# Kernel optimization log

Hardware: AMD Instinct MI355X
Metric: run time of the kernel (lower is better)

The kernel has to match this reference:

```python
import math
import jax, jax.numpy as jnp
import numpy as np

HEAD_DIM = 64


def skew(X):
    # X: (B, M, L). Pad M+1 zeros on last dim, flatten, drop last M, reshape.
    # Shifts row i right by i -> aligns relative positions (adaptive-span trick).
    B, M, L = X.shape
    X = jnp.pad(X, ((0, 0), (0, 0), (0, M + 1)))  # (B, M, L+M+1)
    X = X.reshape(B, -1)[:, :-M].reshape(B, M, M + L)
    return X


def setup_inputs() -> dict:
    key = jax.random.key(0)
    k1, k2, k3, k4 = jax.random.split(key, 4)
    BH, M, D, LIM = 16, 2048, HEAD_DIM, 2048
    return {
        "query": jax.random.normal(k1, (BH, M, D), jnp.float32),
        "key": jax.random.normal(k2, (BH, M, D), jnp.float32),
        "value": jax.random.normal(k3, (BH, M, D), jnp.float32),
        "key_pe": jax.random.normal(k4, (1, D, LIM), jnp.float32),
    }


def reference(query, key, value, key_pe):
    M = query.shape[1]
    Lk = key.shape[1]
    neg_inf = jnp.float32(float("-inf"))
    # causal mask: -inf strictly above diagonal, last M rows
    mask_causal = jnp.triu(jnp.full((Lk, Lk), neg_inf, dtype=query.dtype), k=1)[-M:]
    # content scores: (BH, M, Lk)
    attn = jnp.einsum("bmd,bld->bml", query, key)
    L_size = attn.shape[-1]
    # relative-position scores via skew trick
    attn_pos = jnp.einsum("bmd,xdl->bml", query, key_pe[:, :, -L_size:])
    attn_pos = skew(attn_pos)[:, :, -L_size - 1:-1]
    attn = (attn + attn_pos + mask_causal) / math.sqrt(HEAD_DIM)
    attn = jax.nn.softmax(attn, axis=-1)
    out = jnp.einsum("bml,bld->bmd", attn, value)
    return out  # aux_loss is the constant 0 in the original module
```

## Files before the change

kernel.cpp:

```cpp
#include <hip/hip_runtime.h>
#include <hip/hip_bf16.h>

typedef __attribute__((ext_vector_type(8))) short short8;
typedef __attribute__((ext_vector_type(4))) float f32x4;

#define MFMA16(A, B, C) __builtin_amdgcn_mfma_f32_16x16x32_bf16((A), (B), (C), 0, 0, 0)

#define GL16(gp, lp) __builtin_amdgcn_global_load_lds( \
    (const __attribute__((address_space(1))) void*)(gp), \
    (__attribute__((address_space(3))) void*)(lp), 16, 0, 0)

__device__ __forceinline__ unsigned short bfbits(float f) {
  return __builtin_bit_cast(unsigned short, (__bf16)f);
}

constexpr int BH = 16;
constexpr int Mn = 2048;
constexpr int Dn = 64;
constexpr int LIMn = 2048;
constexpr size_t KF_SHORTS = (size_t)BH * 32 * 8 * 512;
constexpr size_t PE_JROWS = 132;
constexpr size_t PEF_SHORTS = PE_JROWS * 2 * 512;
constexpr int PART_SLOT = 4224;
constexpr int SLOTS_PER_HEAD = 72;

__device__ __forceinline__ int part_offs(int mt) {
  return (mt < 16) ? 2 * (mt - 8) : (mt < 24 ? 16 + 3 * (mt - 16) : 40 + 4 * (mt - 24));
}


__global__ void prep_all(const float* __restrict__ K, const float* __restrict__ V,
                         const float* __restrict__ PE,
                         unsigned short* __restrict__ Kf, unsigned short* __restrict__ Vf,
                         unsigned short* __restrict__ PEf) {
  __shared__ float tA[64 * 64];
  __shared__ float tB[64 * 64];
  const int b = blockIdx.x, tid = threadIdx.x;
  const int w = tid >> 6, lane = tid & 63, g = lane >> 4, q15 = lane & 15;

  if (b < 512) {
    const int bh = b >> 5, lt = b & 31;
    const float* Ks = K + ((size_t)bh * Mn + lt * 64) * Dn;
    const float* Vs = V + ((size_t)bh * Mn + lt * 64) * Dn;
    const int row = tid >> 2, c0 = (tid & 3) * 16;
#pragma unroll
    for (int i = 0; i < 4; ++i) {
      *(float4*)&tA[row * 64 + c0 + 4 * i] = ((const float4*)(Ks + (size_t)row * 64 + c0))[i];
      *(float4*)&tB[row * 64 + c0 + 4 * i] = ((const float4*)(Vs + (size_t)row * 64 + c0))[i];
    }
    __syncthreads();
#pragma unroll
    for (int i = 0; i < 2; ++i) {
      const int f = 2 * w + i, nt = f >> 1, s = f & 1;
      short8 uk, uv;
#pragma unroll
      for (int j = 0; j < 8; ++j) {
        uk[j] = (short)bfbits(tA[(nt * 16 + q15) * 64 + s * 32 + g * 8 + j]);
        uv[j] = (short)bfbits(tB[(s * 32 + g * 8 + j) * 64 + nt * 16 + q15]);
      }
      const size_t base = ((size_t)(bh * 32 + lt) * 8 + f) * 512 + lane * 8;
      *(short8*)&Kf[base] = uk;
      *(short8*)&Vf[base] = uv;
    }
  } else {
    const int pb = b - 512;
    const int c0 = pb * 64;
    const int d = tid >> 2, cc = (tid & 3) * 16;
#pragma unroll
    for (int i = 0; i < 16; ++i) {
      const int c = c0 + cc + i;
      tA[(cc + i) * 64 + d] = (c < LIMn) ? PE[(size_t)d * LIMn + c] : 0.0f;
    }
    __syncthreads();
#pragma unroll
    for (int s = 0; s < 2; ++s) {
      short8 u;
#pragma unroll
      for (int j = 0; j < 8; ++j)
        u[j] = (short)bfbits(tA[(w * 16 + q15) * 64 + s * 32 + g * 8 + j]);
      *(short8*)&PEf[((size_t)(4 * pb + w) * 2 + s) * 512 + lane * 8] = u;
    }
  }
}


__launch_bounds__(256)
__global__ void stair_main(const float* __restrict__ Qg,
                           const unsigned short* __restrict__ Kf,
                           const unsigned short* __restrict__ Vf,
                           const unsigned short* __restrict__ PEf,
                           float* __restrict__ Og,
                           float* __restrict__ Part,
                           int split) {
  __shared__ __align__(16) unsigned short Kbuf[2][2][4096];
  __shared__ __align__(16) unsigned short Vbuf[2][2][4096];
  __shared__ __align__(16) unsigned short Plds[4][2048];

  const int tid = threadIdx.x;
  const int w = tid >> 6, lane = tid & 63, g = lane >> 4, q15 = lane & 15;
  const int bid = blockIdx.x;

  int bh, mt, chunk, t0, t1, nch;
  bh = bid & 15;
  if (split) {
    const int u = bid >> 4;
    if (u < 32)      { mt = 31 - (u >> 2); chunk = u & 3; }
    else if (u < 56) { const int v = u - 32, q = v / 3; mt = 23 - q; chunk = v - q * 3; }
    else if (u < 72) { const int v = u - 56; mt = 15 - (v >> 1); chunk = v & 1; }
    else             { mt = 7 - (u - 72); chunk = 0; }
    t0 = chunk * 8;
    t1 = (t0 + 8 < mt + 1) ? (t0 + 8) : (mt + 1);
    nch = (mt + 8) >> 3;
  } else {
    mt = 31 - (bid >> 4); chunk = 0; t0 = 0; t1 = mt + 1; nch = 1;
  }
  const int m0w = mt * 64 + w * 16;

  const float* Qb = Qg + (size_t)bh * Mn * Dn;
  float* Ob = Og + (size_t)bh * Mn * Dn;

  short8 aq[2];
  {
    const float* qp = Qb + (size_t)(m0w + q15) * Dn;
#pragma unroll
    for (int s = 0; s < 2; ++s) {
      const float4* p = (const float4*)(qp + s * 32 + g * 8);
      float4 f0 = p[0], f1 = p[1];
      short8 a;
      a[0]=(short)bfbits(f0.x); a[1]=(short)bfbits(f0.y); a[2]=(short)bfbits(f0.z); a[3]=(short)bfbits(f0.w);
      a[4]=(short)bfbits(f1.x); a[5]=(short)bfbits(f1.y); a[6]=(short)bfbits(f1.z); a[7]=(short)bfbits(f1.w);
      aq[s] = a;
    }
  }

  float mrun[4], lrun[4];
  f32x4 o[4] = {};
#pragma unroll
  for (int r = 0; r < 4; ++r) { mrun[r] = -1e30f; lrun[r] = 0.0f; }

  auto STAGE1 = [&](int b, int slot, int t) {
    const size_t toff = ((size_t)(bh * 32 + t) * 8) * 512;
#pragma unroll
    for (int i = 0; i < 2; ++i) {
      const int f = 2 * w + i;
      const size_t off = toff + (size_t)f * 512 + lane * 8;
      GL16(&Kf[off], &Kbuf[b][slot][f * 512]);
      GL16(&Vf[off], &Vbuf[b][slot][f * 512]);
    }
  };

  auto QK = [&](f32x4 qk[4], int cur, int slot, int ntmax) {
#pragma unroll
    for (int s = 0; s < 2; ++s)
#pragma unroll
      for (int nt = 0; nt < 4; ++nt)
        if (nt <= ntmax) {
          short8 bfr = *(const short8*)&Kbuf[cur][slot][(nt * 2 + s) * 512 + lane * 8];
          qk[nt] = MFMA16(aq[s], bfr, qk[nt]);
        }
  };

  auto GATHER = [&](float sv[4][4], const f32x4 qk[4], const f32x4 ev[5],
                    int ntmax, bool diag) {
#pragma unroll
    for (int nt = 0; nt < 4; ++nt)
      if (nt <= ntmax) {
#pragma unroll
        for (int r = 0; r < 4; ++r) {
          const int rw = g * 4 + r;
          const int srcLane = (lane & 48) | ((q15 + 15 - rw) & 15);
          float e_lo = __shfl(ev[nt][r], srcLane, 64);
          float e_hi = __shfl(ev[nt + 1][r], srcLane, 64);
          float er = (q15 > rw) ? e_hi : e_lo;
          const int li = nt * 16 + q15;
          bool masked = diag && (li > w * 16 + rw);
          sv[nt][r] = masked ? -1e30f : (qk[nt][r] + er) * 0.125f;
        }
      }
  };

  auto PV = [&](const float sv[4][4], int cur, int slot, int smax) {
#pragma unroll
    for (int nt = 0; nt < 4; ++nt)
#pragma unroll
      for (int r = 0; r < 4; ++r) {
        const int rw = g * 4 + r;
        Plds[w][slot * 1024 + ((rw * 64 + nt * 16 + q15) ^ ((rw & 7) << 3))] = bfbits(sv[nt][r]);
      }
    short8 pa[2];
#pragma unroll
    for (int s = 0; s < 2; ++s)
      if (s <= smax)
        pa[s] = *(short8*)&Plds[w][slot * 1024 + ((q15 * 64 + s * 32 + g * 8) ^ ((q15 & 7) << 3))];
#pragma unroll
    for (int s = 0; s < 2; ++s)
      if (s <= smax)
#pragma unroll
        for (int nt = 0; nt < 4; ++nt) {
          short8 bfr = *(const short8*)&Vbuf[cur][slot][(nt * 2 + s) * 512 + lane * 8];
          o[nt] = MFMA16(pa[s], bfr, o[nt]);
        }
  };

  auto PAIR = [&](int t, int cur, bool diagB) {
    const int jbA = 127 - 4 * mt - w + 4 * t;
    const int jbB = jbA + 4;
    const int ntmaxB = diagB ? w : 3;
    const int u5B = diagB ? (w + 2) : 5;
    const int smaxB = diagB ? (w >> 1) : 1;

    short8 peA[2][5], peB[2][5];
#pragma unroll
    for (int s = 0; s < 2; ++s)
#pragma unroll
      for (int u = 0; u < 5; ++u) {
        peA[s][u] = *(const short8*)&PEf[((size_t)(jbA + u) * 2 + s) * 512 + lane * 8];
        if (u < u5B)
          peB[s][u] = *(const short8*)&PEf[((size_t)(jbB + u) * 2 + s) * 512 + lane * 8];
      }

    f32x4 qkA[4] = {}, qkB[4] = {};
    QK(qkA, cur, 0, 3);
    QK(qkB, cur, 1, ntmaxB);

    f32x4 evA[5] = {};
#pragma unroll
    for (int s = 0; s < 2; ++s)
#pragma unroll
      for (int u = 0; u < 5; ++u) evA[u] = MFMA16(aq[s], peA[s][u], evA[u]);

    float svA[4][4], svB[4][4];
#pragma unroll
    for (int nt = 0; nt < 4; ++nt)
#pragma unroll
      for (int r = 0; r < 4; ++r) { svA[nt][r] = -1e30f; svB[nt][r] = -1e30f; }

    GATHER(svA, qkA, evA, 3, false);

    f32x4 evB[5] = {};
#pragma unroll
    for (int s = 0; s < 2; ++s)
#pragma unroll
      for (int u = 0; u < 5; ++u)
        if (u < u5B) evB[u] = MFMA16(aq[s], peB[s][u], evB[u]);

    GATHER(svB, qkB, evB, ntmaxB, diagB);

    float lmax[4];
#pragma unroll
    for (int r = 0; r < 4; ++r) {
      float a = fmaxf(fmaxf(svA[0][r], svA[1][r]), fmaxf(svA[2][r], svA[3][r]));
      float b = fmaxf(fmaxf(svB[0][r], svB[1][r]), fmaxf(svB[2][r], svB[3][r]));
      lmax[r] = fmaxf(a, b);
    }
    const bool fast = __all((lmax[0] <= mrun[0] + 8.f) & (lmax[1] <= mrun[1] + 8.f) &
                            (lmax[2] <= mrun[2] + 8.f) & (lmax[3] <= mrun[3] + 8.f));
    if (!fast) {
#pragma unroll
      for (int r = 0; r < 4; ++r) {
        float mx = lmax[r];
        mx = fmaxf(mx, __shfl_xor(mx, 1));
        mx = fmaxf(mx, __shfl_xor(mx, 2));
        mx = fmaxf(mx, __shfl_xor(mx, 4));
        mx = fmaxf(mx, __shfl_xor(mx, 8));
        const float mn = fmaxf(mrun[r], mx);
        const float alpha = exp2f((mrun[r] - mn) * 1.44269504f);
        mrun[r] = mn;
        lrun[r] *= alpha;
        o[0][r] *= alpha; o[1][r] *= alpha; o[2][r] *= alpha; o[3][r] *= alpha;
      }
    }
#pragma unroll
    for (int nt = 0; nt < 4; ++nt)
#pragma unroll
      for (int r = 0; r < 4; ++r) {
        svA[nt][r] = exp2f((svA[nt][r] - mrun[r]) * 1.44269504f);
        svB[nt][r] = exp2f((svB[nt][r] - mrun[r]) * 1.44269504f);
      }
#pragma unroll
    for (int r = 0; r < 4; ++r) {
      float sum = ((svA[0][r] + svA[1][r]) + (svA[2][r] + svA[3][r])) +
                  ((svB[0][r] + svB[1][r]) + (svB[2][r] + svB[3][r]));
      sum += __shfl_xor(sum, 1);
      sum += __shfl_xor(sum, 2);
      sum += __shfl_xor(sum, 4);
      sum += __shfl_xor(sum, 8);
      lrun[r] += sum;
    }

    PV(svA, cur, 0, 1);
    PV(svB, cur, 1, smaxB);
  };

  auto SINGLE = [&](int t, int cur, bool diag) {
    const int jb = 127 - 4 * mt - w + 4 * t;
    const int ntmax = diag ? w : 3;
    const int u5 = diag ? (w + 2) : 5;
    const int smax = diag ? (w >> 1) : 1;

    short8 pe[2][5];
#pragma unroll
    for (int s = 0; s < 2; ++s)
#pragma unroll
      for (int u = 0; u < 5; ++u)
        if (u < u5)
          pe[s][u] = *(const short8*)&PEf[((size_t)(jb + u) * 2 + s) * 512 + lane * 8];

    f32x4 qk[4] = {};
    QK(qk, cur, 0, ntmax);
    f32x4 ev[5] = {};
#pragma unroll
    for (int s = 0; s < 2; ++s)
#pragma unroll
      for (int u = 0; u < 5; ++u)
        if (u < u5) ev[u] = MFMA16(aq[s], pe[s][u], ev[u]);

    float sv[4][4];
#pragma unroll
    for (int nt = 0; nt < 4; ++nt)
#pragma unroll
      for (int r = 0; r < 4; ++r) sv[nt][r] = -1e30f;
    GATHER(sv, qk, ev, ntmax, diag);

    float lmax[4];
#pragma unroll
    for (int r = 0; r < 4; ++r)
      lmax[r] = fmaxf(fmaxf(sv[0][r], sv[1][r]), fmaxf(sv[2][r], sv[3][r]));
    const bool fast = __all((lmax[0] <= mrun[0] + 8.f) & (lmax[1] <= mrun[1] + 8.f) &
                            (lmax[2] <= mrun[2] + 8.f) & (lmax[3] <= mrun[3] + 8.f));
    if (!fast) {
#pragma unroll
      for (int r = 0; r < 4; ++r) {
        float mx = lmax[r];
        mx = fmaxf(mx, __shfl_xor(mx, 1));
        mx = fmaxf(mx, __shfl_xor(mx, 2));
        mx = fmaxf(mx, __shfl_xor(mx, 4));
        mx = fmaxf(mx, __shfl_xor(mx, 8));
        const float mn = fmaxf(mrun[r], mx);
        const float alpha = exp2f((mrun[r] - mn) * 1.44269504f);
        mrun[r] = mn;
        lrun[r] *= alpha;
        o[0][r] *= alpha; o[1][r] *= alpha; o[2][r] *= alpha; o[3][r] *= alpha;
      }
    }
#pragma unroll
    for (int nt = 0; nt < 4; ++nt)
#pragma unroll
      for (int r = 0; r < 4; ++r)
        sv[nt][r] = exp2f((sv[nt][r] - mrun[r]) * 1.44269504f);
#pragma unroll
    for (int r = 0; r < 4; ++r) {
      float sum = (sv[0][r] + sv[1][r]) + (sv[2][r] + sv[3][r]);
      sum += __shfl_xor(sum, 1);
      sum += __shfl_xor(sum, 2);
      sum += __shfl_xor(sum, 4);
      sum += __shfl_xor(sum, 8);
      lrun[r] += sum;
    }
    PV(sv, cur, 0, smax);
  };

  {
    int cur = 0;
    int t = t0;
    const int n0 = (t1 - t0 >= 2) ? 2 : 1;
    STAGE1(0, 0, t0);
    if (n0 == 2) STAGE1(0, 1, t0 + 1);
    __syncthreads();
    while (t < t1) {
      const int n = (t1 - t >= 2) ? 2 : 1;
      const int rem = t1 - (t + n);
      const int nn = (rem >= 2) ? 2 : rem;
      if (nn > 0) {
        STAGE1(cur ^ 1, 0, t + n);
        if (nn == 2) STAGE1(cur ^ 1, 1, t + n + 1);
      }
      if (n == 2) PAIR(t, cur, (t + 1 == mt));
      else SINGLE(t, cur, (t == mt));
      if (nn > 0) __syncthreads();
      cur ^= 1;
      t += n;
    }
  }

  if (nch == 1) {
#pragma unroll
    for (int nt = 0; nt < 4; ++nt)
#pragma unroll
      for (int r = 0; r < 4; ++r) {
        const int m = m0w + g * 4 + r;
        Ob[(size_t)m * Dn + nt * 16 + q15] = o[nt][r] / lrun[r];
      }
  } else {
    float* ps = Part + ((size_t)bh * SLOTS_PER_HEAD + part_offs(mt) + chunk) * PART_SLOT;
#pragma unroll
    for (int nt = 0; nt < 4; ++nt)
#pragma unroll
      for (int r = 0; r < 4; ++r)
        ps[(w * 16 + g * 4 + r) * 64 + nt * 16 + q15] = o[nt][r];
#pragma unroll
    for (int r = 0; r < 4; ++r)
      if (q15 == g * 4 + r) {
        ps[4096 + w * 16 + q15] = mrun[r];
        ps[4160 + w * 16 + q15] = lrun[r];
      }
  }
}


__launch_bounds__(256, 4)
__global__ void combine_parts(const float* __restrict__ Part, float* __restrict__ Og) {
  const int bid = blockIdx.x;
  const int bh = bid & 15;
  const int mt = 8 + (bid >> 4);
  const int nch = (mt + 8) >> 3;
  const float* base = Part + ((size_t)bh * SLOTS_PER_HEAD + part_offs(mt)) * PART_SLOT;
  const int tid = threadIdx.x;
  const int row = tid >> 2;
  const int qc = (tid & 3) * 16;

  float mstar = -1e30f;
#pragma unroll
  for (int c = 0; c < 4; ++c)
    if (c < nch) mstar = fmaxf(mstar, base[c * PART_SLOT + 4096 + row]);
  float lsum = 0.f;
  f32x4 acc0 = {}, acc1 = {}, acc2 = {}, acc3 = {};
#pragma unroll
  for (int c = 0; c < 4; ++c)
    if (c < nch) {
      const float* ps = base + c * PART_SLOT;
      const float sc = exp2f((ps[4096 + row] - mstar) * 1.44269504f);
      lsum += ps[4160 + row] * sc;
      const f32x4* op = (const f32x4*)&ps[row * 64 + qc];
      acc0 += op[0] * sc; acc1 += op[1] * sc; acc2 += op[2] * sc; acc3 += op[3] * sc;
    }
  const float inv = 1.f / lsum;
  float* dst = Og + ((size_t)bh * Mn + mt * 64 + row) * Dn + qc;
  *(f32x4*)&dst[0]  = acc0 * inv;
  *(f32x4*)&dst[4]  = acc1 * inv;
  *(f32x4*)&dst[8]  = acc2 * inv;
  *(f32x4*)&dst[12] = acc3 * inv;
}


constexpr int ESTRIDE = 84;

__launch_bounds__(256, 2)
__global__ void stair_attn_fb(const float* __restrict__ Qg,
                              const float* __restrict__ Kg,
                              const float* __restrict__ Vg,
                              const float* __restrict__ PEg,
                              float* __restrict__ Og) {
  __shared__ __align__(16) unsigned short Kb[64 * 64];
  __shared__ __align__(16) unsigned short Vt[64 * 64];
  __shared__ __align__(16) unsigned short Pb[128 * 64];
  __shared__ __align__(16) float Elds[4 * 16 * ESTRIDE];
  __shared__ __align__(16) unsigned short Plds[4 * 16 * 64];

  const int tid = threadIdx.x;
  const int w = tid >> 6;
  const int lane = tid & 63;
  const int g = lane >> 4;
  const int q15 = lane & 15;

  const int bid = blockIdx.x;
  const int bh = bid & 15;
  const int jid = bid >> 4;
  const int mt = (jid < 16) ? (2 * jid) : (63 - 2 * jid);
  const int m0 = mt * 64;

  const float* Qb = Qg + (size_t)bh * Mn * Dn;
  const float* Kbase = Kg + (size_t)bh * Mn * Dn;
  const float* Vbase = Vg + (size_t)bh * Mn * Dn;
  float* Ob = Og + (size_t)bh * Mn * Dn;

  short8 aq[2];
  {
    const float* qp = Qb + (size_t)(m0 + 16 * w + q15) * Dn;
#pragma unroll
    for (int s = 0; s < 2; ++s) {
      const float4* p = (const float4*)(qp + s * 32 + g * 8);
      float4 f0 = p[0], f1 = p[1];
      short8 a;
      a[0]=(short)bfbits(f0.x); a[1]=(short)bfbits(f0.y); a[2]=(short)bfbits(f0.z); a[3]=(short)bfbits(f0.w);
      a[4]=(short)bfbits(f1.x); a[5]=(short)bfbits(f1.y); a[6]=(short)bfbits(f1.z); a[7]=(short)bfbits(f1.w);
      aq[s] = a;
    }
  }

  float mrun[4], lrun[4];
  f32x4 o[4] = {};
#pragma unroll
  for (int r = 0; r < 4; ++r) { mrun[r] = -1e30f; lrun[r] = 0.0f; }

  const int ntiles = mt + 1;
  const int dso = g * 8;

  for (int t = 0; t < ntiles; ++t) {
    const int l0 = t * 64;
    __syncthreads();
    {
      const int l = tid >> 2;
      const int dq = (tid & 3) * 16;
      const float* kp = Kbase + (size_t)(l0 + l) * Dn + dq;
      short8 u0, u1;
      {
        float4 f = ((const float4*)kp)[0];
        u0[0]=(short)bfbits(f.x); u0[1]=(short)bfbits(f.y); u0[2]=(short)bfbits(f.z); u0[3]=(short)bfbits(f.w);
        f = ((const float4*)kp)[1];
        u0[4]=(short)bfbits(f.x); u0[5]=(short)bfbits(f.y); u0[6]=(short)bfbits(f.z); u0[7]=(short)bfbits(f.w);
        f = ((const float4*)kp)[2];
        u1[0]=(short)bfbits(f.x); u1[1]=(short)bfbits(f.y); u1[2]=(short)bfbits(f.z); u1[3]=(short)bfbits(f.w);
        f = ((const float4*)kp)[3];
        u1[4]=(short)bfbits(f.x); u1[5]=(short)bfbits(f.y); u1[6]=(short)bfbits(f.z); u1[7]=(short)bfbits(f.w);
      }
      const int swz = (l & 7) << 3;
      *(short8*)&Kb[(l * 64 + dq) ^ swz] = u0;
      *(short8*)&Kb[(l * 64 + dq + 8) ^ swz] = u1;
    }
    {
      const int lrow = lane;
      const int ds = w * 16;
      const float* vp = Vbase + (size_t)(l0 + lrow) * Dn + ds;
#pragma unroll
      for (int i = 0; i < 4; ++i) {
        float4 f = ((const float4*)vp)[i];
        int c0 = ds + 4 * i;
        Vt[((c0 + 0) * 64 + lrow) ^ (((c0 + 0) & 7) << 3)] = bfbits(f.x);
        Vt[((c0 + 1) * 64 + lrow) ^ (((c0 + 1) & 7) << 3)] = bfbits(f.y);
        Vt[((c0 + 2) * 64 + lrow) ^ (((c0 + 2) & 7) << 3)] = bfbits(f.z);
        Vt[((c0 + 3) * 64 + lrow) ^ (((c0 + 3) & 7) << 3)] = bfbits(f.w);
      }
    }
    {
      const int d = lane;
      const int cc = w * 32;
      const int cb = (2048 - 64) - m0 + l0;
      const float* pp = PEg + (size_t)d * LIMn + (cb + cc);
      if (cb + cc + 31 < LIMn) {
#pragma unroll
        for (int i = 0; i < 8; ++i) {
          float4 f = ((const float4*)pp)[i];
          int c0 = cc + 4 * i;
          Pb[((c0 + 0) * 64 + d) ^ (((c0 + 0) & 7) << 3)] = bfbits(f.x);
          Pb[((c0 + 1) * 64 + d) ^ (((c0 + 1) & 7) << 3)] = bfbits(f.y);
          Pb[((c0 + 2) * 64 + d) ^ (((c0 + 2) & 7) << 3)] = bfbits(f.z);
          Pb[((c0 + 3) * 64 + d) ^ (((c0 + 3) & 7) << 3)] = bfbits(f.w);
        }
      } else {
        for (int i = 0; i < 32; ++i) {
          int cabs = cb + cc + i;
          float f = (cabs < LIMn) ? pp[i] : 0.0f;
          int c0 = cc + i;
          Pb[(c0 * 64 + d) ^ ((c0 & 7) << 3)] = bfbits(f);
        }
      }
    }
    __syncthreads();

    f32x4 qk[4] = {};
#pragma unroll
    for (int s = 0; s < 2; ++s)
#pragma unroll
      for (int nt = 0; nt < 4; ++nt) {
        int l = nt * 16 + q15;
        short8 b = *(short8*)&Kb[(l * 64 + s * 32 + dso) ^ ((l & 7) << 3)];
        qk[nt] = MFMA16(aq[s], b, qk[nt]);
      }

    f32x4 ev[5] = {};
    const int ntb = 3 - w;
#pragma unroll
    for (int s = 0; s < 2; ++s)
#pragma unroll
      for (int u5 = 0; u5 < 5; ++u5) {
        int c = (ntb + u5) * 16 + q15;
        short8 b = *(short8*)&Pb[(c * 64 + s * 32 + dso) ^ ((c & 7) << 3)];
        ev[u5] = MFMA16(aq[s], b, ev[u5]);
      }
    float* Ew = Elds + w * 16 * ESTRIDE;
#pragma unroll
    for (int u5 = 0; u5 < 5; ++u5)
#pragma unroll
      for (int r = 0; r < 4; ++r)
        Ew[(g * 4 + r) * ESTRIDE + u5 * 16 + q15] = ev[u5][r];

    const bool diag = (t == ntiles - 1);
    float sv[4][4];
#pragma unroll
    for (int nt = 0; nt < 4; ++nt) {
      int li = nt * 16 + q15;
#pragma unroll
      for (int r = 0; r < 4; ++r) {
        int rw = g * 4 + r;
        float eread = Ew[rw * ESTRIDE + (15 - rw + li)];
        bool masked = diag && (li > (16 * w + rw));
        sv[nt][r] = masked ? -1e30f : (qk[nt][r] + eread) * 0.125f;
      }
    }

    float mnew[4], alpha[4];
#pragma unroll
    for (int r = 0; r < 4; ++r) {
      float mx = fmaxf(fmaxf(sv[0][r], sv[1][r]), fmaxf(sv[2][r], sv[3][r]));
      mx = fmaxf(mx, __shfl_xor(mx, 1));
      mx = fmaxf(mx, __shfl_xor(mx, 2));
      mx = fmaxf(mx, __shfl_xor(mx, 4));
      mx = fmaxf(mx, __shfl_xor(mx, 8));
      float mn = fmaxf(mrun[r], mx);
      alpha[r] = exp2f((mrun[r] - mn) * 1.44269504f);
      mnew[r] = mn;
      mrun[r] = mn;
    }
    float pexp[4][4];
#pragma unroll
    for (int nt = 0; nt < 4; ++nt)
#pragma unroll
      for (int r = 0; r < 4; ++r)
        pexp[nt][r] = exp2f((sv[nt][r] - mnew[r]) * 1.44269504f);
#pragma unroll
    for (int r = 0; r < 4; ++r) {
      float sum = (pexp[0][r] + pexp[1][r]) + (pexp[2][r] + pexp[3][r]);
      sum += __shfl_xor(sum, 1);
      sum += __shfl_xor(sum, 2);
      sum += __shfl_xor(sum, 4);
      sum += __shfl_xor(sum, 8);
      lrun[r] = lrun[r] * alpha[r] + sum;
      o[0][r] *= alpha[r];
      o[1][r] *= alpha[r];
      o[2][r] *= alpha[r];
      o[3][r] *= alpha[r];
    }

    unsigned short* Pw = Plds + w * 16 * 64;
#pragma unroll
    for (int nt = 0; nt < 4; ++nt)
#pragma unroll
      for (int r = 0; r < 4; ++r) {
        int rw = g * 4 + r;
        Pw[(rw * 64 + nt * 16 + q15) ^ ((rw & 7) << 3)] = bfbits(pexp[nt][r]);
      }
    short8 pa[2];
#pragma unroll
    for (int s = 0; s < 2; ++s)
      pa[s] = *(short8*)&Pw[(q15 * 64 + s * 32 + dso) ^ ((q15 & 7) << 3)];

#pragma unroll
    for (int s = 0; s < 2; ++s)
#pragma unroll
      for (int nt = 0; nt < 4; ++nt) {
        int d = nt * 16 + q15;
        short8 b = *(short8*)&Vt[(d * 64 + s * 32 + dso) ^ ((d & 7) << 3)];
        o[nt] = MFMA16(pa[s], b, o[nt]);
      }
  }

#pragma unroll
  for (int nt = 0; nt < 4; ++nt)
#pragma unroll
    for (int r = 0; r < 4; ++r) {
      int m = m0 + 16 * w + g * 4 + r;
      Ob[(size_t)m * Dn + nt * 16 + q15] = o[nt][r] / lrun[r];
    }
}


extern "C" void kernel_launch(void* const* d_in, const int* in_sizes, int n_in,
                              void* d_out, int out_size, void* d_ws, size_t ws_size,
                              hipStream_t stream) {
  (void)in_sizes; (void)n_in; (void)out_size;
  const float* Q  = (const float*)d_in[0];
  const float* K  = (const float*)d_in[1];
  const float* V  = (const float*)d_in[2];
  const float* PE = (const float*)d_in[3];
  float* Out = (float*)d_out;

  const size_t szK = KF_SHORTS * sizeof(unsigned short);
  const size_t szV = szK;
  const size_t szP = PEF_SHORTS * sizeof(unsigned short);
  const size_t szPart = (size_t)BH * SLOTS_PER_HEAD * PART_SLOT * 4;
  const size_t need1 = szK + szV + szP;
  const size_t need2 = need1 + szPart;

  if (ws_size >= need1) {
    unsigned short* Kf  = (unsigned short*)d_ws;
    unsigned short* Vf  = (unsigned short*)((char*)d_ws + szK);
    unsigned short* PEf = (unsigned short*)((char*)d_ws + szK + szV);
    float* Part = (float*)((char*)d_ws + need1);

    hipLaunchKernelGGL(prep_all, dim3(512 + 33), dim3(256), 0, stream, K, V, PE, Kf, Vf, PEf);
    if (ws_size >= need2) {
      hipLaunchKernelGGL(stair_main, dim3(BH * 80), dim3(256), 0, stream,
                         Q, Kf, Vf, PEf, Out, Part, 1);
      hipLaunchKernelGGL(combine_parts, dim3(BH * 24), dim3(256), 0, stream, Part, Out);
    } else {
      hipLaunchKernelGGL(stair_main, dim3(512), dim3(256), 0, stream,
                         Q, Kf, Vf, PEf, Out, (float*)d_ws, 0);
    }
  } else {
    hipLaunchKernelGGL(stair_attn_fb, dim3(512), dim3(256), 0, stream, Q, K, V, PE, Out);
  }
}
```

Baseline: 78.97 us.

## Load V directly to registers, defer row-sum reduction, and single-shuffle skew gather

V tiles are no longer staged through LDS; each wave loads its V fragments straight from global memory into registers, interleaved with PE loads and compute, which halves the LDS footprint and the Plds buffer. The softmax denominator is kept as a per-lane partial sum and reduced across lanes only once at the end instead of every tile. The gather that aligns relative-position scores now selects the source value before a single shuffle instead of doing two shuffles. This raises register pressure and global-load traffic for V but cuts LDS traffic, shuffles and per-iteration reduction work.

```diff
diff --git a/kernel.cpp b/kernel.cpp
--- a/kernel.cpp
+++ b/kernel.cpp
@@ -93,8 +93,7 @@
                            float* __restrict__ Part,
                            int split) {
   __shared__ __align__(16) unsigned short Kbuf[2][2][4096];
-  __shared__ __align__(16) unsigned short Vbuf[2][2][4096];
-  __shared__ __align__(16) unsigned short Plds[4][2048];
+  __shared__ __align__(16) unsigned short Plds[4][1024];
 
   const int tid = threadIdx.x;
   const int w = tid >> 6, lane = tid & 63, g = lane >> 4, q15 = lane & 15;
@@ -115,6 +114,7 @@
     mt = 31 - (bid >> 4); chunk = 0; t0 = 0; t1 = mt + 1; nch = 1;
   }
   const int m0w = mt * 64 + w * 16;
+  const int jb0 = 127 - 4 * mt - w;
 
   const float* Qb = Qg + (size_t)bh * Mn * Dn;
   float* Ob = Og + (size_t)bh * Mn * Dn;
@@ -133,23 +133,36 @@
     }
   }
 
-  float mrun[4], lrun[4];
+  float mrun[4], lp[4];
   f32x4 o[4] = {};
 #pragma unroll
-  for (int r = 0; r < 4; ++r) { mrun[r] = -1e30f; lrun[r] = 0.0f; }
-
-  auto STAGE1 = [&](int b, int slot, int t) {
+  for (int r = 0; r < 4; ++r) { mrun[r] = -1e30f; lp[r] = 0.0f; }
+
+  auto STAGEK = [&](int b, int slot, int t) {
     const size_t toff = ((size_t)(bh * 32 + t) * 8) * 512;
 #pragma unroll
     for (int i = 0; i < 2; ++i) {
       const int f = 2 * w + i;
-      const size_t off = toff + (size_t)f * 512 + lane * 8;
-      GL16(&Kf[off], &Kbuf[b][slot][f * 512]);
-      GL16(&Vf[off], &Vbuf[b][slot][f * 512]);
-    }
-  };
-
-  auto QK = [&](f32x4 qk[4], int cur, int slot, int ntmax) {
+      GL16(&Kf[toff + (size_t)f * 512 + lane * 8], &Kbuf[b][slot][f * 512]);
+    }
+  };
+
+  auto LOADV = [&](short8 (&vb)[8], int t, int smax) {
+    const size_t base = ((size_t)(bh * 32 + t) * 8) * 512 + (size_t)lane * 8;
+#pragma unroll
+    for (int f = 0; f < 8; ++f)
+      if ((f & 1) <= smax) vb[f] = *(const short8*)&Vf[base + (size_t)f * 512];
+  };
+  auto LOADPE = [&](short8 (&pe)[10], int t, int u5) {
+    const size_t base = ((size_t)((jb0 + 4 * t)) * 2) * 512 + (size_t)lane * 8;
+#pragma unroll
+    for (int i = 0; i < 10; ++i)
+      if ((i >> 1) < u5) pe[i] = *(const short8*)&PEf[base + (size_t)i * 512];
+  };
+
+  auto QK = [&](f32x4 (&qk)[4], int cur, int slot, int ntmax) {
+#pragma unroll
+    for (int nt = 0; nt < 4; ++nt) qk[nt] = f32x4{};
 #pragma unroll
     for (int s = 0; s < 2; ++s)
 #pragma unroll
@@ -159,8 +172,17 @@
           qk[nt] = MFMA16(aq[s], bfr, qk[nt]);
         }
   };
-
-  auto GATHER = [&](float sv[4][4], const f32x4 qk[4], const f32x4 ev[5],
+  auto EB = [&](f32x4 (&ev)[5], const short8 (&pe)[10], int u5) {
+#pragma unroll
+    for (int u = 0; u < 5; ++u) ev[u] = f32x4{};
+#pragma unroll
+    for (int s = 0; s < 2; ++s)
+#pragma unroll
+      for (int u = 0; u < 5; ++u)
+        if (u < u5) ev[u] = MFMA16(aq[s], pe[u * 2 + s], ev[u]);
+  };
+
+  auto GATHER = [&](float sv[4][4], const f32x4 (&qk)[4], const f32x4 (&ev)[5],
                     int ntmax, bool diag) {
 #pragma unroll
     for (int nt = 0; nt < 4; ++nt)
@@ -169,81 +191,67 @@
         for (int r = 0; r < 4; ++r) {
           const int rw = g * 4 + r;
           const int srcLane = (lane & 48) | ((q15 + 15 - rw) & 15);
-          float e_lo = __shfl(ev[nt][r], srcLane, 64);
-          float e_hi = __shfl(ev[nt + 1][r], srcLane, 64);
-          float er = (q15 > rw) ? e_hi : e_lo;
+          const bool cond = (((q15 + rw + 1) & 15) > rw);
+          const float sel = cond ? ev[nt + 1][r] : ev[nt][r];
+          const float er = __shfl(sel, srcLane, 64);
           const int li = nt * 16 + q15;
-          bool masked = diag && (li > w * 16 + rw);
+          const bool masked = diag && (li > w * 16 + rw);
           sv[nt][r] = masked ? -1e30f : (qk[nt][r] + er) * 0.125f;
         }
       }
   };
 
-  auto PV = [&](const float sv[4][4], int cur, int slot, int smax) {
+  auto PV = [&](const float sv[4][4], const short8 (&vb)[8], int smax) {
 #pragma unroll
     for (int nt = 0; nt < 4; ++nt)
 #pragma unroll
       for (int r = 0; r < 4; ++r) {
         const int rw = g * 4 + r;
-        Plds[w][slot * 1024 + ((rw * 64 + nt * 16 + q15) ^ ((rw & 7) << 3))] = bfbits(sv[nt][r]);
+        Plds[w][(rw * 64 + nt * 16 + q15) ^ ((rw & 7) << 3)] = bfbits(sv[nt][r]);
       }
     short8 pa[2];
 #pragma unroll
     for (int s = 0; s < 2; ++s)
       if (s <= smax)
-        pa[s] = *(short8*)&Plds[w][slot * 1024 + ((q15 * 64 + s * 32 + g * 8) ^ ((q15 & 7) << 3))];
+        pa[s] = *(short8*)&Plds[w][(q15 * 64 + s * 32 + g * 8) ^ ((q15 & 7) << 3)];
 #pragma unroll
     for (int s = 0; s < 2; ++s)
       if (s <= smax)
 #pragma unroll
-        for (int nt = 0; nt < 4; ++nt) {
-          short8 bfr = *(const short8*)&Vbuf[cur][slot][(nt * 2 + s) * 512 + lane * 8];
-          o[nt] = MFMA16(pa[s], bfr, o[nt]);
-        }
+        for (int nt = 0; nt < 4; ++nt)
+          o[nt] = MFMA16(pa[s], vb[nt * 2 + s], o[nt]);
   };
 
   auto PAIR = [&](int t, int cur, bool diagB) {
-    const int jbA = 127 - 4 * mt - w + 4 * t;
-    const int jbB = jbA + 4;
     const int ntmaxB = diagB ? w : 3;
     const int u5B = diagB ? (w + 2) : 5;
     const int smaxB = diagB ? (w >> 1) : 1;
 
-    short8 peA[2][5], peB[2][5];
-#pragma unroll
-    for (int s = 0; s < 2; ++s)
-#pragma unroll
-      for (int u = 0; u < 5; ++u) {
-        peA[s][u] = *(const short8*)&PEf[((size_t)(jbA + u) * 2 + s) * 512 + lane * 8];
-        if (u < u5B)
-          peB[s][u] = *(const short8*)&PEf[((size_t)(jbB + u) * 2 + s) * 512 + lane * 8];
-      }
-
-    f32x4 qkA[4] = {}, qkB[4] = {};
+    short8 peA[10], vbA[8];
+    LOADPE(peA, t, 5);
+    LOADV(vbA, t, 1);
+
+    f32x4 qkA[4], evA[5];
     QK(qkA, cur, 0, 3);
+    EB(evA, peA, 5);
+
+    float svA[4][4], svB[4][4];
+#pragma unroll
+    for (int nt = 0; nt < 4; ++nt)
+#pragma unroll
+      for (int r = 0; r < 4; ++r) { svA[nt][r] = -1e30f; svB[nt][r] = -1e30f; }
+
+    short8 peB[10];
+    LOADPE(peB, t + 1, u5B);
+
+    GATHER(svA, qkA, evA, 3, false);
+
+    short8 vbB[8];
+    LOADV(vbB, t + 1, smaxB);
+
+    f32x4 qkB[4], evB[5];
     QK(qkB, cur, 1, ntmaxB);
-
-    f32x4 evA[5] = {};
-#pragma unroll
-    for (int s = 0; s < 2; ++s)
-#pragma unroll
-      for (int u = 0; u < 5; ++u) evA[u] = MFMA16(aq[s], peA[s][u], evA[u]);
-
-    float svA[4][4], svB[4][4];
-#pragma unroll
-    for (int nt = 0; nt < 4; ++nt)
-#pragma unroll
-      for (int r = 0; r < 4; ++r) { svA[nt][r] = -1e30f; svB[nt][r] = -1e30f; }
-
-    GATHER(svA, qkA, evA, 3, false);
-
-    f32x4 evB[5] = {};
-#pragma unroll
-    for (int s = 0; s < 2; ++s)
-#pragma unroll
-      for (int u = 0; u < 5; ++u)
-        if (u < u5B) evB[u] = MFMA16(aq[s], peB[s][u], evB[u]);
-
+    EB(evB, peB, u5B);
     GATHER(svB, qkB, evB, ntmaxB, diagB);
 
     float lmax[4];
@@ -266,7 +274,7 @@
         const float mn = fmaxf(mrun[r], mx);
         const float alpha = exp2f((mrun[r] - mn) * 1.44269504f);
         mrun[r] = mn;
-        lrun[r] *= alpha;
+        lp[r] *= alpha;
         o[0][r] *= alpha; o[1][r] *= alpha; o[2][r] *= alpha; o[3][r] *= alpha;
       }
     }
@@ -278,42 +286,26 @@
         svB[nt][r] = exp2f((svB[nt][r] - mrun[r]) * 1.44269504f);
       }
 #pragma unroll
-    for (int r = 0; r < 4; ++r) {
-      float sum = ((svA[0][r] + svA[1][r]) + (svA[2][r] + svA[3][r])) +
-                  ((svB[0][r] + svB[1][r]) + (svB[2][r] + svB[3][r]));
-      sum += __shfl_xor(sum, 1);
-      sum += __shfl_xor(sum, 2);
-      sum += __shfl_xor(sum, 4);
-      sum += __shfl_xor(sum, 8);
-      lrun[r] += sum;
-    }
-
-    PV(svA, cur, 0, 1);
-    PV(svB, cur, 1, smaxB);
+    for (int r = 0; r < 4; ++r)
+      lp[r] += ((svA[0][r] + svA[1][r]) + (svA[2][r] + svA[3][r])) +
+               ((svB[0][r] + svB[1][r]) + (svB[2][r] + svB[3][r]));
+
+    PV(svA, vbA, 1);
+    PV(svB, vbB, smaxB);
   };
 
   auto SINGLE = [&](int t, int cur, bool diag) {
-    const int jb = 127 - 4 * mt - w + 4 * t;
     const int ntmax = diag ? w : 3;
     const int u5 = diag ? (w + 2) : 5;
     const int smax = diag ? (w >> 1) : 1;
 
-    short8 pe[2][5];
-#pragma unroll
-    for (int s = 0; s < 2; ++s)
-#pragma unroll
-      for (int u = 0; u < 5; ++u)
-        if (u < u5)
-          pe[s][u] = *(const short8*)&PEf[((size_t)(jb + u) * 2 + s) * 512 + lane * 8];
-
-    f32x4 qk[4] = {};
+    short8 pe[10], vb[8];
+    LOADPE(pe, t, u5);
+    LOADV(vb, t, smax);
+
+    f32x4 qk[4], ev[5];
     QK(qk, cur, 0, ntmax);
-    f32x4 ev[5] = {};
-#pragma unroll
-    for (int s = 0; s < 2; ++s)
-#pragma unroll
-      for (int u = 0; u < 5; ++u)
-        if (u < u5) ev[u] = MFMA16(aq[s], pe[s][u], ev[u]);
+    EB(ev, pe, u5);
 
     float sv[4][4];
 #pragma unroll
@@ -339,7 +331,7 @@
         const float mn = fmaxf(mrun[r], mx);
         const float alpha = exp2f((mrun[r] - mn) * 1.44269504f);
         mrun[r] = mn;
-        lrun[r] *= alpha;
+        lp[r] *= alpha;
         o[0][r] *= alpha; o[1][r] *= alpha; o[2][r] *= alpha; o[3][r] *= alpha;
       }
     }
@@ -349,31 +341,26 @@
       for (int r = 0; r < 4; ++r)
         sv[nt][r] = exp2f((sv[nt][r] - mrun[r]) * 1.44269504f);
 #pragma unroll
-    for (int r = 0; r < 4; ++r) {
-      float sum = (sv[0][r] + sv[1][r]) + (sv[2][r] + sv[3][r]);
-      sum += __shfl_xor(sum, 1);
-      sum += __shfl_xor(sum, 2);
-      sum += __shfl_xor(sum, 4);
-      sum += __shfl_xor(sum, 8);
-      lrun[r] += sum;
-    }
-    PV(sv, cur, 0, smax);
+    for (int r = 0; r < 4; ++r)
+      lp[r] += (sv[0][r] + sv[1][r]) + (sv[2][r] + sv[3][r]);
+
+    PV(sv, vb, smax);
   };
 
   {
     int cur = 0;
     int t = t0;
     const int n0 = (t1 - t0 >= 2) ? 2 : 1;
-    STAGE1(0, 0, t0);
-    if (n0 == 2) STAGE1(0, 1, t0 + 1);
+    STAGEK(0, 0, t0);
+    if (n0 == 2) STAGEK(0, 1, t0 + 1);
     __syncthreads();
     while (t < t1) {
       const int n = (t1 - t >= 2) ? 2 : 1;
       const int rem = t1 - (t + n);
       const int nn = (rem >= 2) ? 2 : rem;
       if (nn > 0) {
-        STAGE1(cur ^ 1, 0, t + n);
-        if (nn == 2) STAGE1(cur ^ 1, 1, t + n + 1);
+        STAGEK(cur ^ 1, 0, t + n);
+        if (nn == 2) STAGEK(cur ^ 1, 1, t + n + 1);
       }
       if (n == 2) PAIR(t, cur, (t + 1 == mt));
       else SINGLE(t, cur, (t == mt));
@@ -383,13 +370,24 @@
     }
   }
 
+  float lr[4];
+#pragma unroll
+  for (int r = 0; r < 4; ++r) {
+    float s = lp[r];
+    s += __shfl_xor(s, 1);
+    s += __shfl_xor(s, 2);
+    s += __shfl_xor(s, 4);
+    s += __shfl_xor(s, 8);
+    lr[r] = s;
+  }
+
   if (nch == 1) {
 #pragma unroll
     for (int nt = 0; nt < 4; ++nt)
 #pragma unroll
       for (int r = 0; r < 4; ++r) {
         const int m = m0w + g * 4 + r;
-        Ob[(size_t)m * Dn + nt * 16 + q15] = o[nt][r] / lrun[r];
+        Ob[(size_t)m * Dn + nt * 16 + q15] = o[nt][r] / lr[r];
       }
   } else {
     float* ps = Part + ((size_t)bh * SLOTS_PER_HEAD + part_offs(mt) + chunk) * PART_SLOT;
@@ -402,7 +400,7 @@
     for (int r = 0; r < 4; ++r)
       if (q15 == g * 4 + r) {
         ps[4096 + w * 16 + q15] = mrun[r];
-        ps[4160 + w * 16 + q15] = lrun[r];
+        ps[4160 + w * 16 + q15] = lr[r];
       }
   }
 }
```

New measurement: 105.2 us. 1.33x slower.
